# Kernel optimization log

Measured on AMD Instinct MI355X. Metric: run time of the kernel, lower is better.

Reference implementation:

```python
import jax, jax.numpy as jnp
import numpy as np

N_NODES = 50000
N_EDGES = 600000
DIM = 128
HEADS = 8
HEAD_DIM = DIM // HEADS  # 16


def leaky(x, slope=0.01):
    return jnp.where(x >= 0, x, slope * x)


def gat_layer(x, W, a_src, a_dst, bias, src, dst):
    # x: [N, DIM]; W: [DIM, DIM]; a_src/a_dst: [HEADS, HEAD_DIM]; bias: [DIM]
    N = x.shape[0]
    xh = (x @ W).reshape(N, HEADS, HEAD_DIM)
    alpha_src = jnp.sum(xh * a_src, axis=-1)  # [N, H]
    alpha_dst = jnp.sum(xh * a_dst, axis=-1)  # [N, H]
    e = leaky(alpha_src[src] + alpha_dst[dst], 0.2)  # [E, H], PyG negative_slope=0.2
    # segment softmax over edges sharing the same destination node
    e_max = jax.ops.segment_max(e, dst, num_segments=N)
    ex = jnp.exp(e - e_max[dst])
    denom = jax.ops.segment_sum(ex, dst, num_segments=N)
    alpha = ex / (denom[dst] + 1e-16)
    out = jax.ops.segment_sum(xh[src] * alpha[:, :, None], dst, num_segments=N)
    return out.reshape(N, DIM) + bias


def setup_inputs() -> dict:
    key = jax.random.key(0)
    ks = jax.random.split(key, 20)
    s_d = 1.0 / np.sqrt(DIM)
    s_h = 1.0 / np.sqrt(DIM // 2)
    inp = {
        'features': jax.random.normal(ks[0], (N_NODES, DIM), jnp.float32),
        'edge_index': jax.random.randint(ks[1], (2, N_EDGES), 0, N_NODES, jnp.int64)
            if jax.config.jax_enable_x64 else
            jax.random.randint(ks[1], (2, N_EDGES), 0, N_NODES).astype(jnp.int32),
        'W1': jax.random.normal(ks[2], (DIM, DIM), jnp.float32) * s_d,
        'a_src1': jax.random.normal(ks[3], (HEADS, HEAD_DIM), jnp.float32) * s_d,
        'a_dst1': jax.random.normal(ks[4], (HEADS, HEAD_DIM), jnp.float32) * s_d,
        'b1': jnp.zeros((DIM,), jnp.float32),
        'W2': jax.random.normal(ks[5], (DIM, DIM), jnp.float32) * s_d,
        'a_src2': jax.random.normal(ks[6], (HEADS, HEAD_DIM), jnp.float32) * s_d,
        'a_dst2': jax.random.normal(ks[7], (HEADS, HEAD_DIM), jnp.float32) * s_d,
        'b2': jnp.zeros((DIM,), jnp.float32),
        'wm1': jax.random.normal(ks[8], (DIM, DIM // 2), jnp.float32) * s_d,
        'bm1': jnp.zeros((DIM // 2,), jnp.float32),
        'wm2': jax.random.normal(ks[9], (DIM // 2, 1), jnp.float32) * s_h,
        'bm2': jnp.zeros((1,), jnp.float32),
        'wa1': jax.random.normal(ks[10], (DIM, DIM // 2), jnp.float32) * s_d,
        'ba1': jnp.zeros((DIM // 2,), jnp.float32),
        'wa2': jax.random.normal(ks[11], (DIM // 2, DIM), jnp.float32) * s_h,
        'ba2': jnp.zeros((DIM,), jnp.float32),
        'gamma': jnp.ones((DIM,), jnp.float32),
        'beta': jnp.zeros((DIM,), jnp.float32),
    }
    return inp


def reference(features, edge_index, W1, a_src1, a_dst1, b1, W2, a_src2, a_dst2, b2,
              wm1, bm1, wm2, bm2, wa1, ba1, wa2, ba2, gamma, beta):
    N = features.shape[0]
    loops = jnp.arange(N, dtype=edge_index.dtype)
    src = jnp.concatenate([edge_index[0], loops])  # PyG add_self_loops=True
    dst = jnp.concatenate([edge_index[1], loops])
    h = leaky(gat_layer(features, W1, a_src1, a_dst1, b1, src, dst))
    h = leaky(gat_layer(h, W2, a_src2, a_dst2, b2, src, dst))
    scores = (leaky(h @ wm1 + bm1) @ wm2 + bm2)[:, 0]  # [N]
    w = jax.nn.softmax(scores, axis=0)
    agg = jnp.sum(w[:, None] * h, axis=0)  # [DIM]
    z = leaky(agg @ wa1 + ba1) @ wa2 + ba2
    mu = jnp.mean(z)
    var = jnp.mean((z - mu) ** 2)
    return gamma * (z - mu) / jnp.sqrt(var + 1e-5) + beta
```

## Files before the change

kernel.cpp:

```cpp
#include <hip/hip_runtime.h>
#include <math.h>

#define DIM 128
#define HEADS 8
#define HD 16
#define CAP 64

typedef __attribute__((ext_vector_type(8))) short s16x8;
typedef __attribute__((ext_vector_type(8))) unsigned short u16x8;
typedef __attribute__((ext_vector_type(4))) float f32x4;

__device__ __forceinline__ float lrelu(float x, float s) { return x >= 0.f ? x : s * x; }

__device__ __forceinline__ unsigned short f2bf(float x) {
  unsigned u = __float_as_uint(x);
  return (unsigned short)((u + 0x7FFFu + ((u >> 16) & 1u)) >> 16);
}
__device__ __forceinline__ float bf2f(unsigned short b) {
  return __uint_as_float(((unsigned)b) << 16);
}

__global__ void k_hist(const int* __restrict__ ei, int E, int N, int* __restrict__ cnt) {
  int tot = E + N;
  for (int i = blockIdx.x * blockDim.x + threadIdx.x; i < tot; i += gridDim.x * blockDim.x) {
    int d = (i < E) ? ei[E + i] : (i - E);
    atomicAdd(&cnt[d], 1);
  }
}

__global__ __launch_bounds__(256) void k_scan_blk(const int* __restrict__ cnt, int n,
                                                  int* __restrict__ excl, int* __restrict__ bsum) {
  __shared__ int wsum[4];
  int tid = threadIdx.x, l = tid & 63, w = tid >> 6;
  int i = blockIdx.x * 256 + tid;
  int v = (i < n) ? cnt[i] : 0;
  int s = v;
#pragma unroll
  for (int off = 1; off < 64; off <<= 1) {
    int t = __shfl_up(s, off, 64);
    if (l >= off) s += t;
  }
  if (l == 63) wsum[w] = s;
  __syncthreads();
  int add = 0;
#pragma unroll
  for (int k = 0; k < 4; ++k) add += (k < w) ? wsum[k] : 0;
  if (i < n) excl[i] = s + add - v;
  if (tid == 255) bsum[blockIdx.x] = s + add;
}

__global__ __launch_bounds__(256) void k_scan_top(const int* __restrict__ bsum, int nb,
                                                  int* __restrict__ boff, int* __restrict__ rowptrN) {
  __shared__ int wsum[4];
  int tid = threadIdx.x, l = tid & 63, w = tid >> 6;
  int v = (tid < nb) ? bsum[tid] : 0;
  int s = v;
#pragma unroll
  for (int off = 1; off < 64; off <<= 1) {
    int t = __shfl_up(s, off, 64);
    if (l >= off) s += t;
  }
  if (l == 63) wsum[w] = s;
  __syncthreads();
  int add = 0;
#pragma unroll
  for (int k = 0; k < 4; ++k) add += (k < w) ? wsum[k] : 0;
  if (tid < nb) boff[tid] = s + add - v;
  if (tid == 255) *rowptrN = s + add;
}

__global__ __launch_bounds__(256) void k_scan_fix(int* __restrict__ cursor, const int* __restrict__ boff,
                                                  int n, int* __restrict__ rowptr) {
  int i = blockIdx.x * 256 + threadIdx.x;
  if (i < n) {
    int r = boff[blockIdx.x] + cursor[i];
    rowptr[i] = r;
    cursor[i] = r;
  }
}

__global__ __launch_bounds__(256) void k_prep(
    const float* __restrict__ W1, const float* __restrict__ as1, const float* __restrict__ ad1,
    const float* __restrict__ W2, const float* __restrict__ as2, const float* __restrict__ ad2,
    const float* __restrict__ wm1,
    unsigned short* __restrict__ wh1,
    unsigned short* __restrict__ sh1, unsigned short* __restrict__ sl1,
    unsigned short* __restrict__ wh2,
    unsigned short* __restrict__ sh2, unsigned short* __restrict__ sl2,
    unsigned short* __restrict__ mh, unsigned short* __restrict__ ml,
    int* __restrict__ cnt, int N) {
  int b = blockIdx.x, tid = threadIdx.x;
  if (b < 32) {
    int layer = b >> 4;
    const float* W = layer ? W2 : W1;
    unsigned short* wh = layer ? wh2 : wh1;
    int lo = (b & 15) * 1024;
    for (int idx = lo + tid; idx < lo + 1024; idx += 256) {
      int n = idx >> 7, k = idx & 127;
      wh[idx] = f2bf(W[k * DIM + n]);
    }
  } else if (b < 36) {
    int layer = (b - 32) >> 1;
    const float* W = layer ? W2 : W1;
    const float* avs = layer ? as2 : as1;
    const float* avd = layer ? ad2 : ad1;
    unsigned short* sh = layer ? sh2 : sh1;
    unsigned short* sl = layer ? sl2 : sl1;
    int lo = ((b - 32) & 1) * 1024;
    for (int idx = lo + tid; idx < lo + 1024; idx += 256) {
      int n = idx >> 7, k = idx & 127;
      float acc = 0.f;
      if (n < 8) {
#pragma unroll
        for (int j = 0; j < 16; ++j) acc += W[k * DIM + n * 16 + j] * avs[n * 16 + j];
      } else {
        int h = n - 8;
#pragma unroll
        for (int j = 0; j < 16; ++j) acc += W[k * DIM + h * 16 + j] * avd[h * 16 + j];
      }
      unsigned short hb = f2bf(acc);
      sh[idx] = hb;
      sl[idx] = f2bf(acc - bf2f(hb));
    }
  } else if (b < 44) {
    int lo = (b - 36) * 1024;
    for (int idx = lo + tid; idx < lo + 1024; idx += 256) {
      int j = idx >> 7, k = idx & 127;
      float v = wm1[k * 64 + j];
      unsigned short hb = f2bf(v);
      mh[idx] = hb;
      ml[idx] = f2bf(v - bf2f(hb));
    }
  } else {
    int i0 = (b - 44) * 2048 + tid * 8;
    if (i0 + 8 <= N) {
      int4 z = {0, 0, 0, 0};
      *(int4*)(cnt + i0) = z;
      *(int4*)(cnt + i0 + 4) = z;
    } else {
      for (int i = i0; i < N; ++i) cnt[i] = 0;
    }
  }
}

template <int BF16IN, int FUSE>
__global__ __launch_bounds__(256) void k_linear_mfma(
    const void* __restrict__ xin,
    const unsigned short* __restrict__ wh,
    const unsigned short* __restrict__ sh, const unsigned short* __restrict__ sl,
    unsigned short* __restrict__ xhb, float* __restrict__ asrc, float* __restrict__ adst,
    int N, int GL,
    const int* __restrict__ ei, int E, int* __restrict__ cursor, int* __restrict__ colb) {
  if constexpr (FUSE == 1) {
    if ((int)blockIdx.x >= GL) {
      int tot = E + N;
      int nsb = gridDim.x - GL;
      for (int i = ((int)blockIdx.x - GL) * 256 + (int)threadIdx.x; i < tot; i += nsb * 256) {
        int s, d;
        if (i < E) { s = ei[i]; d = ei[E + i]; } else { s = i - E; d = s; }
        int pos = atomicAdd(&cursor[d], 1);
        colb[pos] = s;
      }
      return;
    }
  }
  __shared__ unsigned short sB[160][136];
  __shared__ unsigned short otile[64][136];
  __shared__ float atile[64][16];
  int tid = threadIdx.x, l = tid & 63, w = tid >> 6;
  int g = l >> 4, c = l & 15;
  int rb = blockIdx.x * 64;

  for (int i = tid; i < 160 * 16; i += 256) {
    int row = i >> 4, c8 = i & 15;
    u16x8 v;
    if (row < 128) v = *(const u16x8*)(wh + row * 128 + c8 * 8);
    else if (row < 144) v = *(const u16x8*)(sh + (row - 128) * 128 + c8 * 8);
    else v = *(const u16x8*)(sl + (row - 144) * 128 + c8 * 8);
    *(u16x8*)&sB[row][c8 * 8] = v;
  }

  int rc = min(rb + w * 16 + c, N - 1);
  s16x8 A[4];
  if constexpr (BF16IN) {
    const s16x8* xr = (const s16x8*)((const unsigned short*)xin + (size_t)rc * DIM);
#pragma unroll
    for (int kt = 0; kt < 4; ++kt) A[kt] = xr[kt * 4 + g];
  } else {
    const float4* xf = (const float4*)((const float*)xin + (size_t)rc * DIM);
#pragma unroll
    for (int kt = 0; kt < 4; ++kt) {
      float4 p = xf[kt * 8 + g * 2];
      float4 q = xf[kt * 8 + g * 2 + 1];
      s16x8 a;
      a[0] = (short)f2bf(p.x); a[1] = (short)f2bf(p.y);
      a[2] = (short)f2bf(p.z); a[3] = (short)f2bf(p.w);
      a[4] = (short)f2bf(q.x); a[5] = (short)f2bf(q.y);
      a[6] = (short)f2bf(q.z); a[7] = (short)f2bf(q.w);
      A[kt] = a;
    }
  }
  __syncthreads();

  f32x4 acc[8];
#pragma unroll
  for (int ct = 0; ct < 8; ++ct) acc[ct] = (f32x4){0.f, 0.f, 0.f, 0.f};
#pragma unroll
  for (int kt = 0; kt < 4; ++kt) {
    s16x8 a = A[kt];
#pragma unroll
    for (int ct = 0; ct < 8; ++ct) {
      s16x8 b = *(const s16x8*)&sB[ct * 16 + c][kt * 32 + g * 8];
      acc[ct] = __builtin_amdgcn_mfma_f32_16x16x32_bf16(a, b, acc[ct], 0, 0, 0);
    }
  }
  f32x4 accS = {0.f, 0.f, 0.f, 0.f};
#pragma unroll
  for (int kt = 0; kt < 4; ++kt) {
    s16x8 shi = *(const s16x8*)&sB[128 + c][kt * 32 + g * 8];
    s16x8 slo = *(const s16x8*)&sB[144 + c][kt * 32 + g * 8];
    accS = __builtin_amdgcn_mfma_f32_16x16x32_bf16(A[kt], shi, accS, 0, 0, 0);
    accS = __builtin_amdgcn_mfma_f32_16x16x32_bf16(A[kt], slo, accS, 0, 0, 0);
  }

#pragma unroll
  for (int ct = 0; ct < 8; ++ct)
#pragma unroll
    for (int r = 0; r < 4; ++r)
      otile[w * 16 + g * 4 + r][ct * 16 + c] = f2bf(acc[ct][r]);
#pragma unroll
  for (int r = 0; r < 4; ++r) atile[w * 16 + g * 4 + r][c] = accS[r];
  __syncthreads();

#pragma unroll
  for (int p = 0; p < 4; ++p) {
    int row = p * 16 + (tid >> 4), cb = tid & 15;
    int rr = rb + row;
    if (rr < N) {
      u16x8 v = *(const u16x8*)&otile[row][cb * 8];
      *(u16x8*)(xhb + (size_t)rr * DIM + cb * 8) = v;
      float av = atile[row][cb];
      if (cb < 8) asrc[rr * HEADS + cb] = av;
      else adst[rr * HEADS + (cb - 8)] = av;
    }
  }
}

__global__ __launch_bounds__(256) void k_gat_agg(const int* __restrict__ rowptr, const int* __restrict__ colb,
                                                 const unsigned short* __restrict__ xhb,
                                                 const float* __restrict__ asrc, const float* __restrict__ adst,
                                                 const float* __restrict__ bias,
                                                 unsigned short* __restrict__ houtb, int N) {
  __shared__ int ci[4][CAP];
  int tid = threadIdx.x, lane = tid & 63, wv = tid >> 6;
  int n = blockIdx.x * 4 + wv;
  int base = 0, deg = 0;
  if (n < N) { base = rowptr[n]; deg = rowptr[n + 1] - base; }
  if (lane < deg && lane < CAP) ci[wv][lane] = colb[base + lane];
  __syncthreads();
  if (n >= N) return;

  int qt = lane >> 4, q = lane & 15;
  int h = q >> 1;
  float adn = adst[n * HEADS + h];
  float den = 0.f;
  float a0 = 0.f, a1 = 0.f, a2 = 0.f, a3 = 0.f, a4 = 0.f, a5 = 0.f, a6 = 0.f, a7 = 0.f;
#define EDGE(ii) { \
    int c_ = ((ii) < CAP) ? ci[wv][(ii)] : colb[base + (ii)]; \
    float e_ = lrelu(asrc[c_ * HEADS + h] + adn, 0.2f); \
    float w_ = __expf(e_); \
    den += w_; \
    u16x8 u_ = *(const u16x8*)(xhb + (size_t)c_ * DIM + q * 8); \
    a0 = fmaf(w_, bf2f((unsigned short)u_[0]), a0); \
    a1 = fmaf(w_, bf2f((unsigned short)u_[1]), a1); \
    a2 = fmaf(w_, bf2f((unsigned short)u_[2]), a2); \
    a3 = fmaf(w_, bf2f((unsigned short)u_[3]), a3); \
    a4 = fmaf(w_, bf2f((unsigned short)u_[4]), a4); \
    a5 = fmaf(w_, bf2f((unsigned short)u_[5]), a5); \
    a6 = fmaf(w_, bf2f((unsigned short)u_[6]), a6); \
    a7 = fmaf(w_, bf2f((unsigned short)u_[7]), a7); }
  int i = qt;
  for (; i + 4 < deg; i += 8) { EDGE(i); EDGE(i + 4); }
  for (; i < deg; i += 4) { EDGE(i); }
#undef EDGE
  den += __shfl_xor(den, 16, 64); den += __shfl_xor(den, 32, 64);
  a0 += __shfl_xor(a0, 16, 64); a0 += __shfl_xor(a0, 32, 64);
  a1 += __shfl_xor(a1, 16, 64); a1 += __shfl_xor(a1, 32, 64);
  a2 += __shfl_xor(a2, 16, 64); a2 += __shfl_xor(a2, 32, 64);
  a3 += __shfl_xor(a3, 16, 64); a3 += __shfl_xor(a3, 32, 64);
  a4 += __shfl_xor(a4, 16, 64); a4 += __shfl_xor(a4, 32, 64);
  a5 += __shfl_xor(a5, 16, 64); a5 += __shfl_xor(a5, 32, 64);
  a6 += __shfl_xor(a6, 16, 64); a6 += __shfl_xor(a6, 32, 64);
  a7 += __shfl_xor(a7, 16, 64); a7 += __shfl_xor(a7, 32, 64);
  if (qt == 0) {
    float r = 1.f / (den + 1e-16f);
    const float4* bp = (const float4*)(bias + q * 8);
    float4 b0 = bp[0], b1 = bp[1];
    u16x8 o;
    o[0] = f2bf(lrelu(fmaf(a0, r, b0.x), 0.01f));
    o[1] = f2bf(lrelu(fmaf(a1, r, b0.y), 0.01f));
    o[2] = f2bf(lrelu(fmaf(a2, r, b0.z), 0.01f));
    o[3] = f2bf(lrelu(fmaf(a3, r, b0.w), 0.01f));
    o[4] = f2bf(lrelu(fmaf(a4, r, b1.x), 0.01f));
    o[5] = f2bf(lrelu(fmaf(a5, r, b1.y), 0.01f));
    o[6] = f2bf(lrelu(fmaf(a6, r, b1.z), 0.01f));
    o[7] = f2bf(lrelu(fmaf(a7, r, b1.w), 0.01f));
    *(u16x8*)(houtb + (size_t)n * DIM + q * 8) = o;
  }
}

__global__ __launch_bounds__(256) void k_score_pool(
    const unsigned short* __restrict__ h2b,
    const unsigned short* __restrict__ mh, const unsigned short* __restrict__ ml,
    const float* __restrict__ bm1, const float* __restrict__ wm2, const float* __restrict__ bm2,
    float* __restrict__ pagg, float* __restrict__ psum, int N) {
  __shared__ float se[4][16];
  __shared__ float blkacc[4][128];
  __shared__ float swave[4];
  int tid = threadIdx.x, l = tid & 63, w = tid >> 6;
  int g = l >> 4, c = l & 15;
  int rbase = blockIdx.x * 64 + w * 16;
  int rc = min(rbase + c, N - 1);
  const s16x8* xr = (const s16x8*)(h2b + (size_t)rc * DIM);
  s16x8 A[4];
#pragma unroll
  for (int kt = 0; kt < 4; ++kt) A[kt] = xr[kt * 4 + g];

  const s16x8* Bh = (const s16x8*)mh;
  const s16x8* Bl = (const s16x8*)ml;
  float v[4] = {0.f, 0.f, 0.f, 0.f};
#pragma unroll
  for (int ct = 0; ct < 4; ++ct) {
    f32x4 acc = {0.f, 0.f, 0.f, 0.f};
#pragma unroll
    for (int kt = 0; kt < 4; ++kt) {
      s16x8 bh = Bh[(ct * 16 + c) * 16 + kt * 4 + g];
      s16x8 bl = Bl[(ct * 16 + c) * 16 + kt * 4 + g];
      acc = __builtin_amdgcn_mfma_f32_16x16x32_bf16(A[kt], bh, acc, 0, 0, 0);
      acc = __builtin_amdgcn_mfma_f32_16x16x32_bf16(A[kt], bl, acc, 0, 0, 0);
    }
    int col = ct * 16 + c;
    float b = bm1[col], w2 = wm2[col];
#pragma unroll
    for (int r = 0; r < 4; ++r) v[r] += lrelu(acc[r] + b, 0.01f) * w2;
  }
#pragma unroll
  for (int r = 0; r < 4; ++r) {
    v[r] += __shfl_xor(v[r], 1, 64);
    v[r] += __shfl_xor(v[r], 2, 64);
    v[r] += __shfl_xor(v[r], 4, 64);
    v[r] += __shfl_xor(v[r], 8, 64);
  }
  float b2 = bm2[0];
  float e[4];
#pragma unroll
  for (int r = 0; r < 4; ++r) {
    int rr = rbase + g * 4 + r;
    e[r] = (rr < N) ? __expf(v[r] + b2) : 0.f;
  }
  if (c == 0) {
#pragma unroll
    for (int r = 0; r < 4; ++r) se[w][g * 4 + r] = e[r];
  }
  __syncthreads();
  float emy = se[w][c];
  float pa[32];
#pragma unroll
  for (int kt = 0; kt < 4; ++kt)
#pragma unroll
    for (int j = 0; j < 8; ++j)
      pa[kt * 8 + j] = emy * bf2f((unsigned short)A[kt][j]);
#pragma unroll
  for (int k = 0; k < 32; ++k) {
    pa[k] += __shfl_xor(pa[k], 1, 64);
    pa[k] += __shfl_xor(pa[k], 2, 64);
    pa[k] += __shfl_xor(pa[k], 4, 64);
    pa[k] += __shfl_xor(pa[k], 8, 64);
  }
  if (c == 0) {
#pragma unroll
    for (int kt = 0; kt < 4; ++kt)
#pragma unroll
      for (int j = 0; j < 8; ++j)
        blkacc[w][kt * 32 + g * 8 + j] = pa[kt * 8 + j];
  }
  float ws = e[0] + e[1] + e[2] + e[3];
  ws += __shfl_xor(ws, 16, 64);
  ws += __shfl_xor(ws, 32, 64);
  if (l == 0) swave[w] = ws;
  __syncthreads();
  if (tid < 128) {
    float s = blkacc[0][tid] + blkacc[1][tid] + blkacc[2][tid] + blkacc[3][tid];
    pagg[(size_t)blockIdx.x * DIM + tid] = s;
  }
  if (tid == 0) psum[blockIdx.x] = swave[0] + swave[1] + swave[2] + swave[3];
}

__global__ __launch_bounds__(1024) void k_final(const float* __restrict__ psum, const float* __restrict__ pagg,
                                                int nb,
                                                const float* __restrict__ wa1, const float* __restrict__ ba1,
                                                const float* __restrict__ wa2, const float* __restrict__ ba2,
                                                const float* __restrict__ gamma, const float* __restrict__ beta,
                                                float* __restrict__ out) {
  __shared__ float redz[1024];
  __shared__ float reda[8][128];
  __shared__ float sa[128], shh[64], red[128];
  int t = threadIdx.x;
  float zp = 0.f;
  for (int b = t; b < nb; b += 1024) zp += psum[b];
  redz[t] = zp;
  __syncthreads();
  for (int st = 512; st > 0; st >>= 1) { if (t < st) redz[t] += redz[t + st]; __syncthreads(); }
  int d = t & 127, g = t >> 7;
  float ag = 0.f;
  for (int b = g; b < nb; b += 8) ag += pagg[(size_t)b * DIM + d];
  reda[g][d] = ag;
  __syncthreads();
  if (g == 0) {
    float s = 0.f;
#pragma unroll
    for (int k = 0; k < 8; ++k) s += reda[k][d];
    sa[d] = s / redz[0];
  }
  __syncthreads();
  if (t < 64) {
    float a = 0.f;
    for (int k = 0; k < 128; ++k) a = fmaf(sa[k], wa1[k * 64 + t], a);
    a += ba1[t];
    shh[t] = lrelu(a, 0.01f);
  }
  __syncthreads();
  float zval = 0.f;
  if (t < 128) {
    zval = ba2[t];
    for (int j = 0; j < 64; ++j) zval = fmaf(shh[j], wa2[j * 128 + t], zval);
    red[t] = zval;
  }
  __syncthreads();
  for (int st = 64; st > 0; st >>= 1) { if (t < st) red[t] += red[t + st]; __syncthreads(); }
  float mu = red[0] / 128.f;
  __syncthreads();
  if (t < 128) red[t] = (zval - mu) * (zval - mu);
  __syncthreads();
  for (int st = 64; st > 0; st >>= 1) { if (t < st) red[t] += red[t + st]; __syncthreads(); }
  float var = red[0] / 128.f;
  if (t < 128) out[t] = gamma[t] * (zval - mu) / sqrtf(var + 1e-5f) + beta[t];
}

extern "C" void kernel_launch(void* const* d_in, const int* in_sizes, int n_in,
                              void* d_out, int out_size, void* d_ws, size_t ws_size,
                              hipStream_t stream) {
  const float* feat = (const float*)d_in[0];
  const int* ei = (const int*)d_in[1];
  const float* W1 = (const float*)d_in[2];
  const float* as1 = (const float*)d_in[3];
  const float* ad1 = (const float*)d_in[4];
  const float* b1 = (const float*)d_in[5];
  const float* W2 = (const float*)d_in[6];
  const float* as2 = (const float*)d_in[7];
  const float* ad2 = (const float*)d_in[8];
  const float* b2 = (const float*)d_in[9];
  const float* wm1 = (const float*)d_in[10];
  const float* bm1 = (const float*)d_in[11];
  const float* wm2 = (const float*)d_in[12];
  const float* bm2 = (const float*)d_in[13];
  const float* wa1 = (const float*)d_in[14];
  const float* ba1 = (const float*)d_in[15];
  const float* wa2 = (const float*)d_in[16];
  const float* ba2 = (const float*)d_in[17];
  const float* gamma = (const float*)d_in[18];
  const float* beta = (const float*)d_in[19];
  float* out = (float*)d_out;

  int N = in_sizes[0] / DIM;
  int E = in_sizes[1] / 2;
  int NB = (N + 255) / 256;
  int ZB = (N + 2047) / 2048;
  int GL = (N + 63) / 64;
  int GS = 448;
  int gs = (N + 63) / 64;

  char* ws = (char*)d_ws;
  size_t off = 0;
  auto alloc = [&](size_t bytes) -> void* {
    void* p = ws + off;
    off = (off + bytes + 255) & ~(size_t)255;
    return p;
  };
  int* cnt = (int*)alloc((size_t)N * 4);
  int* rowptr = (int*)alloc((size_t)(N + 1) * 4);
  int* cursor = (int*)alloc((size_t)N * 4);
  int* colb = (int*)alloc((size_t)(E + N) * 4);
  unsigned short* xhb = (unsigned short*)alloc((size_t)N * DIM * 2);
  unsigned short* h1b = (unsigned short*)alloc((size_t)N * DIM * 2);
  unsigned short* h2b = (unsigned short*)alloc((size_t)N * DIM * 2);
  float* asrcb = (float*)alloc((size_t)N * HEADS * 4);
  float* adstb = (float*)alloc((size_t)N * HEADS * 4);
  float* pagg = (float*)alloc((size_t)gs * DIM * 4);
  float* psum = (float*)alloc((size_t)gs * 4);
  int* bsum = (int*)alloc((size_t)NB * 4);
  int* boff = (int*)alloc((size_t)NB * 4);
  unsigned short* wh1 = (unsigned short*)alloc(DIM * DIM * 2);
  unsigned short* sh1 = (unsigned short*)alloc(16 * DIM * 2);
  unsigned short* sl1 = (unsigned short*)alloc(16 * DIM * 2);
  unsigned short* wh2 = (unsigned short*)alloc(DIM * DIM * 2);
  unsigned short* sh2 = (unsigned short*)alloc(16 * DIM * 2);
  unsigned short* sl2 = (unsigned short*)alloc(16 * DIM * 2);
  unsigned short* mh = (unsigned short*)alloc(64 * DIM * 2);
  unsigned short* ml = (unsigned short*)alloc(64 * DIM * 2);

  k_prep<<<44 + ZB, 256, 0, stream>>>(W1, as1, ad1, W2, as2, ad2, wm1,
                                      wh1, sh1, sl1, wh2, sh2, sl2, mh, ml, cnt, N);

  k_hist<<<1024, 256, 0, stream>>>(ei, E, N, cnt);
  k_scan_blk<<<NB, 256, 0, stream>>>(cnt, N, cursor, bsum);
  k_scan_top<<<1, 256, 0, stream>>>(bsum, NB, boff, rowptr + N);
  k_scan_fix<<<NB, 256, 0, stream>>>(cursor, boff, N, rowptr);

  k_linear_mfma<0, 1><<<GL + GS, 256, 0, stream>>>(feat, wh1, sh1, sl1, xhb, asrcb, adstb,
                                                   N, GL, ei, E, cursor, colb);

  int ga = (N + 3) / 4;
  k_gat_agg<<<ga, 256, 0, stream>>>(rowptr, colb, xhb, asrcb, adstb, b1, h1b, N);
  k_linear_mfma<1, 0><<<GL, 256, 0, stream>>>(h1b, wh2, sh2, sl2, xhb, asrcb, adstb,
                                              N, GL, nullptr, 0, nullptr, nullptr);
  k_gat_agg<<<ga, 256, 0, stream>>>(rowptr, colb, xhb, asrcb, adstb, b2, h2b, N);

  k_score_pool<<<gs, 256, 0, stream>>>(h2b, mh, ml, bm1, wm2, bm2, pagg, psum, N);
  k_final<<<1, 1024, 0, stream>>>(psum, pagg, gs, wa1, ba1, wa2, ba2, gamma, beta, out);
}
```

Measured before the change: 225.7 us.

## Split GAT aggregation per head across blocks and drop LDS-staged linear epilogue

```diff
diff --git a/kernel.cpp b/kernel.cpp
--- a/kernel.cpp
+++ b/kernel.cpp
@@ -165,8 +165,6 @@
     }
   }
   __shared__ unsigned short sB[160][136];
-  __shared__ unsigned short otile[64][136];
-  __shared__ float atile[64][16];
   int tid = threadIdx.x, l = tid & 63, w = tid >> 6;
   int g = l >> 4, c = l & 15;
   int rb = blockIdx.x * 64;
@@ -224,24 +222,14 @@
   }
 
 #pragma unroll
-  for (int ct = 0; ct < 8; ++ct)
-#pragma unroll
-    for (int r = 0; r < 4; ++r)
-      otile[w * 16 + g * 4 + r][ct * 16 + c] = f2bf(acc[ct][r]);
-#pragma unroll
-  for (int r = 0; r < 4; ++r) atile[w * 16 + g * 4 + r][c] = accS[r];
-  __syncthreads();
-
-#pragma unroll
-  for (int p = 0; p < 4; ++p) {
-    int row = p * 16 + (tid >> 4), cb = tid & 15;
-    int rr = rb + row;
+  for (int r = 0; r < 4; ++r) {
+    int rr = rb + w * 16 + g * 4 + r;
     if (rr < N) {
-      u16x8 v = *(const u16x8*)&otile[row][cb * 8];
-      *(u16x8*)(xhb + (size_t)rr * DIM + cb * 8) = v;
-      float av = atile[row][cb];
-      if (cb < 8) asrc[rr * HEADS + cb] = av;
-      else adst[rr * HEADS + (cb - 8)] = av;
+#pragma unroll
+      for (int ct = 0; ct < 8; ++ct)
+        xhb[(size_t)rr * DIM + ct * 16 + c] = f2bf(acc[ct][r]);
+      if (c < 8) asrc[rr * HEADS + c] = accS[r];
+      else adst[rr * HEADS + (c - 8)] = accS[r];
     }
   }
 }
@@ -253,59 +241,38 @@
                                                  unsigned short* __restrict__ houtb, int N) {
   __shared__ int ci[4][CAP];
   int tid = threadIdx.x, lane = tid & 63, wv = tid >> 6;
-  int n = blockIdx.x * 4 + wv;
-  int base = 0, deg = 0;
-  if (n < N) { base = rowptr[n]; deg = rowptr[n + 1] - base; }
-  if (lane < deg && lane < CAP) ci[wv][lane] = colb[base + lane];
-  __syncthreads();
-  if (n >= N) return;
-
-  int qt = lane >> 4, q = lane & 15;
-  int h = q >> 1;
-  float adn = adst[n * HEADS + h];
-  float den = 0.f;
-  float a0 = 0.f, a1 = 0.f, a2 = 0.f, a3 = 0.f, a4 = 0.f, a5 = 0.f, a6 = 0.f, a7 = 0.f;
+  int s = blockIdx.x & 7;
+  int n0 = (blockIdx.x >> 3) * 16 + wv * 4;
+  int e = lane >> 4, d = lane & 15;
+  float bv = bias[s * HD + d];
+
+#pragma unroll
+  for (int k = 0; k < 4; ++k) {
+    int n = n0 + k;
+    if (n >= N) break;
+    int base = rowptr[n];
+    int deg = rowptr[n + 1] - base;
+    if (lane < deg && lane < CAP) ci[wv][lane] = colb[base + lane];
+    float adn = adst[n * HEADS + s];
+    float den = 0.f, acc = 0.f;
 #define EDGE(ii) { \
-    int c_ = ((ii) < CAP) ? ci[wv][(ii)] : colb[base + (ii)]; \
-    float e_ = lrelu(asrc[c_ * HEADS + h] + adn, 0.2f); \
-    float w_ = __expf(e_); \
-    den += w_; \
-    u16x8 u_ = *(const u16x8*)(xhb + (size_t)c_ * DIM + q * 8); \
-    a0 = fmaf(w_, bf2f((unsigned short)u_[0]), a0); \
-    a1 = fmaf(w_, bf2f((unsigned short)u_[1]), a1); \
-    a2 = fmaf(w_, bf2f((unsigned short)u_[2]), a2); \
-    a3 = fmaf(w_, bf2f((unsigned short)u_[3]), a3); \
-    a4 = fmaf(w_, bf2f((unsigned short)u_[4]), a4); \
-    a5 = fmaf(w_, bf2f((unsigned short)u_[5]), a5); \
-    a6 = fmaf(w_, bf2f((unsigned short)u_[6]), a6); \
-    a7 = fmaf(w_, bf2f((unsigned short)u_[7]), a7); }
-  int i = qt;
-  for (; i + 4 < deg; i += 8) { EDGE(i); EDGE(i + 4); }
-  for (; i < deg; i += 4) { EDGE(i); }
+      int c_ = ((ii) < CAP) ? ci[wv][(ii)] : colb[base + (ii)]; \
+      float e_ = lrelu(asrc[c_ * HEADS + s] + adn, 0.2f); \
+      float w_ = __expf(e_); \
+      den += w_; \
+      acc = fmaf(w_, bf2f(xhb[(size_t)c_ * DIM + s * HD + d]), acc); }
+    int i = e;
+    for (; i + 4 < deg; i += 8) { EDGE(i); EDGE(i + 4); }
+    for (; i < deg; i += 4) { EDGE(i); }
 #undef EDGE
-  den += __shfl_xor(den, 16, 64); den += __shfl_xor(den, 32, 64);
-  a0 += __shfl_xor(a0, 16, 64); a0 += __shfl_xor(a0, 32, 64);
-  a1 += __shfl_xor(a1, 16, 64); a1 += __shfl_xor(a1, 32, 64);
-  a2 += __shfl_xor(a2, 16, 64); a2 += __shfl_xor(a2, 32, 64);
-  a3 += __shfl_xor(a3, 16, 64); a3 += __shfl_xor(a3, 32, 64);
-  a4 += __shfl_xor(a4, 16, 64); a4 += __shfl_xor(a4, 32, 64);
-  a5 += __shfl_xor(a5, 16, 64); a5 += __shfl_xor(a5, 32, 64);
-  a6 += __shfl_xor(a6, 16, 64); a6 += __shfl_xor(a6, 32, 64);
-  a7 += __shfl_xor(a7, 16, 64); a7 += __shfl_xor(a7, 32, 64);
-  if (qt == 0) {
-    float r = 1.f / (den + 1e-16f);
-    const float4* bp = (const float4*)(bias + q * 8);
-    float4 b0 = bp[0], b1 = bp[1];
-    u16x8 o;
-    o[0] = f2bf(lrelu(fmaf(a0, r, b0.x), 0.01f));
-    o[1] = f2bf(lrelu(fmaf(a1, r, b0.y), 0.01f));
-    o[2] = f2bf(lrelu(fmaf(a2, r, b0.z), 0.01f));
-    o[3] = f2bf(lrelu(fmaf(a3, r, b0.w), 0.01f));
-    o[4] = f2bf(lrelu(fmaf(a4, r, b1.x), 0.01f));
-    o[5] = f2bf(lrelu(fmaf(a5, r, b1.y), 0.01f));
-    o[6] = f2bf(lrelu(fmaf(a6, r, b1.z), 0.01f));
-    o[7] = f2bf(lrelu(fmaf(a7, r, b1.w), 0.01f));
-    *(u16x8*)(houtb + (size_t)n * DIM + q * 8) = o;
+    den += __shfl_xor(den, 16, 64);
+    den += __shfl_xor(den, 32, 64);
+    acc += __shfl_xor(acc, 16, 64);
+    acc += __shfl_xor(acc, 32, 64);
+    if (e == 0) {
+      float r = 1.f / (den + 1e-16f);
+      houtb[(size_t)n * DIM + s * HD + d] = f2bf(lrelu(fmaf(acc, r, bv), 0.01f));
+    }
   }
 }
 
@@ -479,6 +446,7 @@
   int GL = (N + 63) / 64;
   int GS = 448;
   int gs = (N + 63) / 64;
+  int ga = ((N + 15) / 16) * 8;
 
   char* ws = (char*)d_ws;
   size_t off = 0;
@@ -520,7 +488,6 @@
   k_linear_mfma<0, 1><<<GL + GS, 256, 0, stream>>>(feat, wh1, sh1, sl1, xhb, asrcb, adstb,
                                                    N, GL, ei, E, cursor, colb);
 
-  int ga = (N + 3) / 4;
   k_gat_agg<<<ga, 256, 0, stream>>>(rowptr, colb, xhb, asrcb, adstb, b1, h1b, N);
   k_linear_mfma<1, 0><<<GL, 256, 0, stream>>>(h1b, wh2, sh2, sl2, xhb, asrcb, adstb,
                                               N, GL, nullptr, 0, nullptr, nullptr);
```

After: 455.3 us. +101.7%, slower.
